# Kernel tuning notes

Hardware: AMD Instinct MI355X
Metric: run time of the kernel (lower is better)

The kernel has to match this reference:

```python
import jax, jax.numpy as jnp
import numpy as np

B, T, EMB_D, HEAD = 8, 2048, 1024, 128


def setup_inputs() -> dict:
    key = jax.random.key(0)
    ks = jax.random.split(key, 7)
    s = 1.0 / np.sqrt(EMB_D)
    return {
        "inputs": jax.random.normal(ks[0], (B, T, EMB_D), dtype=jnp.float32),
        "Wk": jax.random.uniform(ks[1], (EMB_D, HEAD), jnp.float32, -s, s),
        "bk": jax.random.uniform(ks[2], (HEAD,), jnp.float32, -s, s),
        "Wq": jax.random.uniform(ks[3], (EMB_D, HEAD), jnp.float32, -s, s),
        "bq": jax.random.uniform(ks[4], (HEAD,), jnp.float32, -s, s),
        "Wv": jax.random.uniform(ks[5], (EMB_D, HEAD), jnp.float32, -s, s),
        "bv": jax.random.uniform(ks[6], (HEAD,), jnp.float32, -s, s),
    }


def reference(inputs, Wk, bk, Wq, bq, Wv, bv):
    # inputs: [B, T, C]
    Bq, Tq, _ = inputs.shape
    k = inputs @ Wk + bk  # [B, T, H]
    q = inputs @ Wq + bq
    v = inputs @ Wv + bv
    scale = HEAD ** -0.5
    weights = jnp.einsum("bth,bsh->bts", q, k) * scale  # [B, T, T]
    causal = jnp.tril(jnp.ones((Tq, Tq), dtype=bool))
    weights = jnp.where(causal, weights, -jnp.inf)
    # NOTE: original code applies softmax over dim=1 (the query axis), faithfully reproduced
    weights = jax.nn.softmax(weights, axis=1)
    return jnp.einsum("bts,bsh->bth", weights, v)  # [B, T, H]
```

## Files before the change

kernel.cpp:

```cpp
#include <hip/hip_runtime.h>
#include <hip/hip_bf16.h>

#define T_SEQ 2048
#define NBATCH 8
#define EMB 1024
#define HD 128

typedef _Float16 f16_t;
typedef _Float16 f16x8 __attribute__((ext_vector_type(8)));
typedef _Float16 f16x4 __attribute__((ext_vector_type(4)));
typedef float f32x4 __attribute__((ext_vector_type(4)));


__device__ __forceinline__ void g2l(const f16_t* g, f16_t* l) {
    __builtin_amdgcn_global_load_lds(
        (const __attribute__((address_space(1))) unsigned int*)g,
        (__attribute__((address_space(3))) unsigned int*)l, 16, 0, 0);
}

__global__ __launch_bounds__(256) void prep(
    const float* __restrict__ Wk, const float* __restrict__ bk,
    const float* __restrict__ Wq, const float* __restrict__ bq,
    const float* __restrict__ Wv, const float* __restrict__ bv,
    f16_t* __restrict__ w2, float* __restrict__ biasc,
    float4* __restrict__ out4, float4* __restrict__ colsum4) {
    int bid = blockIdx.x;
    int t = threadIdx.x;
    if (bid < 384) {
        int n = bid;
        const float scale = 0.08838834764831845f;
        const float* W; const float* bias; float sc; int col;
        if (n < 128)      { W = Wq; bias = bq; sc = scale; col = n; }
        else if (n < 256) { W = Wk; bias = bk; sc = 1.0f;  col = n - 128; }
        else              { W = Wv; bias = bv; sc = 1.0f;  col = n - 256; }
        if (t < 128) {
            int k0 = t * 8;
            f16x8 v;
            #pragma unroll
            for (int i = 0; i < 8; ++i) v[i] = (f16_t)(W[(size_t)(k0 + i) * HD + col] * sc);
            *(f16x8*)&w2[(size_t)(n >> 4) * 16384 + (size_t)(k0 >> 3) * 128 + (n & 15) * 8] = v;
        }
        if (t == 0) biasc[n] = bias[col] * sc;
    } else if (bid < 384 + 2048) {
        out4[(size_t)(bid - 384) * 256 + t] = make_float4(0.f, 0.f, 0.f, 0.f);
    } else {
        colsum4[(size_t)(bid - 2432) * 256 + t] = make_float4(0.f, 0.f, 0.f, 0.f);
    }
}

__global__ __launch_bounds__(256) void qkv_gemm(
    const float* __restrict__ X, const f16_t* __restrict__ w2,
    const float* __restrict__ biasc,
    f16_t* __restrict__ q2, f16_t* __restrict__ k2, f16_t* __restrict__ v2) {
    __shared__ f16_t Xs[64 * 72];

    int bid = blockIdx.x;
    int r8 = bid & 7, g = bid >> 3;
    int band = (g / 3) * 8 + r8;
    int i = g % 3;
    int m0 = band * 64, n0 = i * 128;
    int tid = threadIdx.x;
    int lane = tid & 63, w = tid >> 6;
    int quad = lane >> 4, l15 = lane & 15;
    int msub = (w & 1) * 32, nsub = (w >> 1) * 64;

    int srow = tid >> 2;
    int scg  = (tid & 3) * 16;

    const float* xrow = X + (size_t)(m0 + srow) * EMB + scg;

    f32x4 acc[2][4] = {};
    float4 pfA[4], pfB[4];
    #pragma unroll
    for (int u = 0; u < 4; ++u) pfA[u] = *(const float4*)(xrow + u * 4);
    #pragma unroll
    for (int u = 0; u < 4; ++u) pfB[u] = *(const float4*)(xrow + 64 + u * 4);

    auto stage = [&](float4 (&pf)[4]) {
        union { f16_t h[8]; uint4 u4; } p0, p1;
        p0.h[0] = (f16_t)pf[0].x; p0.h[1] = (f16_t)pf[0].y;
        p0.h[2] = (f16_t)pf[0].z; p0.h[3] = (f16_t)pf[0].w;
        p0.h[4] = (f16_t)pf[1].x; p0.h[5] = (f16_t)pf[1].y;
        p0.h[6] = (f16_t)pf[1].z; p0.h[7] = (f16_t)pf[1].w;
        p1.h[0] = (f16_t)pf[2].x; p1.h[1] = (f16_t)pf[2].y;
        p1.h[2] = (f16_t)pf[2].z; p1.h[3] = (f16_t)pf[2].w;
        p1.h[4] = (f16_t)pf[3].x; p1.h[5] = (f16_t)pf[3].y;
        p1.h[6] = (f16_t)pf[3].z; p1.h[7] = (f16_t)pf[3].w;
        *(uint4*)&Xs[srow * 72 + scg] = p0.u4;
        *(uint4*)&Xs[srow * 72 + scg + 8] = p1.u4;
    };
    auto compute = [&](int kc) {
        #pragma unroll
        for (int ks = 0; ks < 2; ++ks) {
            f16x8 afr0 = *(const f16x8*)&Xs[(msub + l15) * 72 + ks * 32 + quad * 8];
            f16x8 afr1 = *(const f16x8*)&Xs[(msub + 16 + l15) * 72 + ks * 32 + quad * 8];
            #pragma unroll
            for (int nf = 0; nf < 4; ++nf) {
                int ntile = (n0 + nsub + nf * 16) >> 4;
                f16x8 bfr = *(const f16x8*)&w2[(size_t)ntile * 16384 +
                    (size_t)((kc >> 3) + ks * 4 + quad) * 128 + l15 * 8];
                acc[0][nf] = __builtin_amdgcn_mfma_f32_16x16x32_f16(afr0, bfr, acc[0][nf], 0, 0, 0);
                acc[1][nf] = __builtin_amdgcn_mfma_f32_16x16x32_f16(afr1, bfr, acc[1][nf], 0, 0, 0);
            }
        }
    };

    for (int it = 0; it < 16; it += 2) {
        __syncthreads();
        stage(pfA);
        __syncthreads();
        if (it + 2 < 16) {
            #pragma unroll
            for (int u = 0; u < 4; ++u) pfA[u] = *(const float4*)(xrow + (it + 2) * 64 + u * 4);
        }
        compute(it * 64);

        __syncthreads();
        stage(pfB);
        __syncthreads();
        if (it + 3 < 16) {
            #pragma unroll
            for (int u = 0; u < 4; ++u) pfB[u] = *(const float4*)(xrow + (it + 3) * 64 + u * 4);
        }
        compute((it + 1) * 64);
    }

    #pragma unroll
    for (int nf = 0; nf < 4; ++nf) {
        int ng = n0 + nsub + nf * 16 + l15;
        float bval = biasc[ng];
        #pragma unroll
        for (int mf = 0; mf < 2; ++mf) {
            int rowg = m0 + msub + mf * 16 + quad * 4;
            f32x4 a = acc[mf][nf];
            if (ng < 256) {
                f16_t* dst = (ng < 128) ? q2 : k2;
                int c = ng & 127;
                #pragma unroll
                for (int r = 0; r < 4; ++r) {
                    int row = rowg + r;
                    dst[(size_t)(row >> 4) * 2048 + (c >> 3) * 128 + (row & 15) * 8 + (c & 7)]
                        = (f16_t)(a[r] + bval);
                }
            } else {
                int h = ng - 256;
                f16x4 hv;
                #pragma unroll
                for (int r = 0; r < 4; ++r) hv[r] = (f16_t)(a[r] + bval);
                *(f16x4*)&v2[(size_t)(rowg >> 3) * 1024 + h * 8 + (rowg & 7)] = hv;
            }
        }
    }
}

__global__ __launch_bounds__(256, 4) void col_stats(
    const f16_t* __restrict__ q2, const f16_t* __restrict__ k2,
    float* __restrict__ colsum) {
    __shared__ __align__(16) f16_t Ql[4 * 2048];

    int bid = blockIdx.x;
    int b = bid & 7;
    int item = 143 - (bid >> 3);
    int cg = 0, slab = 0, cum = 0;
    for (int c = 0; c < 32; ++c) {
        int n = (32 - c + 3) >> 2;
        if (item < cum + n) { cg = c; slab = item - cum; break; }
        cum += n;
    }
    int tc0 = cg + slab * 4, tc1 = min(tc0 + 4, 32);

    int tid = threadIdx.x, lane = tid & 63, w = tid >> 6;
    int quad = lane >> 4, l15 = lane & 15;
    int brow = b * 128;
    size_t base = (size_t)b * T_SEQ;

    f16x8 bfrs[4][4];
    #pragma unroll
    for (int st = 0; st < 4; ++st) {
        const f16_t* kt = k2 + (size_t)(brow + cg * 4 + st) * 2048 + l15 * 8;
        #pragma unroll
        for (int kf = 0; kf < 4; ++kf)
            bfrs[st][kf] = *(const f16x8*)(kt + (kf * 4 + quad) * 128);
    }

    float lacc[4] = {0.f, 0.f, 0.f, 0.f};

    for (int tc = tc0; tc < tc1; ++tc) {
        int tb = tc * 64;
        __syncthreads();
        const f16_t* qsrc = q2 + (size_t)(brow + tc * 4) * 2048;
        #pragma unroll
        for (int i = 0; i < 4; ++i)
            g2l(qsrc + i * 2048 + tid * 8, Ql + i * 2048 + tid * 8);
        __syncthreads();

        f16x8 afr[4];
        #pragma unroll
        for (int kf = 0; kf < 4; ++kf)
            afr[kf] = *(const f16x8*)&Ql[w * 2048 + (kf * 4 + quad) * 128 + l15 * 8];
        #pragma unroll
        for (int st = 0; st < 4; ++st) {
            f32x4 s = {};
            #pragma unroll
            for (int kf = 0; kf < 4; ++kf)
                s = __builtin_amdgcn_mfma_f32_16x16x32_f16(afr[kf], bfrs[st][kf], s, 0, 0, 0);
            int scol = cg * 64 + st * 16 + l15;
            #pragma unroll
            for (int r = 0; r < 4; ++r) {
                int t = tb + w * 16 + quad * 4 + r;
                if (t >= scol) lacc[st] += __expf(s[r]);
            }
        }
    }

    #pragma unroll
    for (int st = 0; st < 4; ++st) {
        float v = lacc[st];
        v += __shfl_xor(v, 16, 64);
        v += __shfl_xor(v, 32, 64);
        if (quad == 0) atomicAdd(&colsum[base + cg * 64 + st * 16 + l15], v);
    }
}

__global__ __launch_bounds__(256, 4) void attn_out(
    const f16_t* __restrict__ q2, const f16_t* __restrict__ k2,
    const f16_t* __restrict__ v2, const float* __restrict__ colsum,
    float* __restrict__ out) {
    __shared__ __align__(16) f16_t Kl[4 * 2048];
    __shared__ __align__(16) f16_t Vl[8 * 1024];
    __shared__ __align__(16) f16_t Pl[32 * 72];

    int bid = blockIdx.x;
    int b = bid & 7;
    int item = 159 - (bid >> 3);
    int g = 0, slab = 0, cum = 0;
    for (int gg = 0; gg < 64; ++gg) {
        int n = (((gg >> 1) + 1) + 7) >> 3;
        if (item < cum + n) { g = gg; slab = item - cum; break; }
        cum += n;
    }
    int nch = (g >> 1) + 1;
    int c0 = slab * 8, c1 = min(c0 + 8, nch);
    int trow = g * 32;

    int tid = threadIdx.x, lane = tid & 63, w = tid >> 6;
    int quad = lane >> 4, l15 = lane & 15;
    int brow = b * 128;
    size_t base = (size_t)b * T_SEQ;

    f16x8 qfr[2][4];
    #pragma unroll
    for (int tt = 0; tt < 2; ++tt) {
        const f16_t* qt = q2 + (size_t)(brow + 2 * g + tt) * 2048 + l15 * 8;
        #pragma unroll
        for (int kf = 0; kf < 4; ++kf)
            qfr[tt][kf] = *(const f16x8*)(qt + (kf * 4 + quad) * 128);
    }

    f32x4 o[2][2] = {};

    for (int c = c0; c < c1; ++c) {
        int sb = c * 64;
        __syncthreads();
        const f16_t* ksrc = k2 + (size_t)(brow + (sb >> 4)) * 2048;
        const f16_t* vsrc = v2 + (((size_t)base + sb) >> 3) * 1024;
        #pragma unroll
        for (int i = 0; i < 4; ++i) {
            g2l(ksrc + i * 2048 + tid * 8, Kl + i * 2048 + tid * 8);
            g2l(vsrc + i * 2048 + tid * 8, Vl + i * 2048 + tid * 8);
        }
        __syncthreads();

        float iv = 1.0f / colsum[base + sb + w * 16 + l15];
        int scol = sb + w * 16 + l15;
        f16x8 bfr[4];
        #pragma unroll
        for (int kf = 0; kf < 4; ++kf)
            bfr[kf] = *(const f16x8*)&Kl[w * 2048 + (kf * 4 + quad) * 128 + l15 * 8];
        #pragma unroll
        for (int tt = 0; tt < 2; ++tt) {
            f32x4 s = {};
            #pragma unroll
            for (int kf = 0; kf < 4; ++kf)
                s = __builtin_amdgcn_mfma_f32_16x16x32_f16(qfr[tt][kf], bfr[kf], s, 0, 0, 0);
            #pragma unroll
            for (int r = 0; r < 4; ++r) {
                int t = trow + tt * 16 + quad * 4 + r;
                float pv = (t >= scol) ? __expf(s[r]) * iv : 0.f;
                Pl[(tt * 16 + quad * 4 + r) * 72 + w * 16 + l15] = (f16_t)pv;
            }
        }
        __syncthreads();

        #pragma unroll
        for (int kf2 = 0; kf2 < 2; ++kf2) {
            f16x8 pa0 = *(const f16x8*)&Pl[(l15) * 72 + kf2 * 32 + quad * 8];
            f16x8 pa1 = *(const f16x8*)&Pl[(16 + l15) * 72 + kf2 * 32 + quad * 8];
            #pragma unroll
            for (int hh = 0; hh < 2; ++hh) {
                f16x8 vfr = *(const f16x8*)&Vl[(kf2 * 4 + quad) * 1024 + (w * 32 + hh * 16 + l15) * 8];
                o[0][hh] = __builtin_amdgcn_mfma_f32_16x16x32_f16(pa0, vfr, o[0][hh], 0, 0, 0);
                o[1][hh] = __builtin_amdgcn_mfma_f32_16x16x32_f16(pa1, vfr, o[1][hh], 0, 0, 0);
            }
        }
    }

    #pragma unroll
    for (int tt = 0; tt < 2; ++tt)
        #pragma unroll
        for (int hh = 0; hh < 2; ++hh)
            #pragma unroll
            for (int r = 0; r < 4; ++r)
                atomicAdd(&out[(base + trow + tt * 16 + quad * 4 + r) * HD + w * 32 + hh * 16 + l15],
                          o[tt][hh][r]);
}

extern "C" void kernel_launch(void* const* d_in, const int* in_sizes, int n_in,
                              void* d_out, int out_size, void* d_ws, size_t ws_size,
                              hipStream_t stream) {
    const float* X  = (const float*)d_in[0];
    const float* Wk = (const float*)d_in[1];
    const float* bk = (const float*)d_in[2];
    const float* Wq = (const float*)d_in[3];
    const float* bq = (const float*)d_in[4];
    const float* Wv = (const float*)d_in[5];
    const float* bv = (const float*)d_in[6];
    float* out = (float*)d_out;

    char* ws = (char*)d_ws;
    const size_t W2_B    = 24 * 16384 * 2;
    const size_t BIAS_B  = 2048;
    const size_t QKV_B   = (size_t)NBATCH * T_SEQ * HD * 2;
    f16_t* w2     = (f16_t*)ws;
    float* biasc  = (float*)(ws + W2_B);
    f16_t* q2     = (f16_t*)(ws + W2_B + BIAS_B);
    f16_t* k2     = (f16_t*)(ws + W2_B + BIAS_B + QKV_B);
    f16_t* v2     = (f16_t*)(ws + W2_B + BIAS_B + 2 * QKV_B);
    float* colsum = (float*)(ws + W2_B + BIAS_B + 3 * QKV_B);

    prep<<<dim3(2448), dim3(256), 0, stream>>>(Wk, bk, Wq, bq, Wv, bv, w2, biasc,
                                               (float4*)out, (float4*)colsum);
    qkv_gemm<<<dim3(768), dim3(256), 0, stream>>>(X, w2, biasc, q2, k2, v2);
    col_stats<<<dim3(1152), dim3(256), 0, stream>>>(q2, k2, colsum);
    attn_out<<<dim3(1280), dim3(256), 0, stream>>>(q2, k2, v2, colsum, out);
}
```

Measured before the change: 176.1 us.

## Stream fp32 X tiles via direct global-to-LDS loads with XOR swizzle and double buffering

After: 177.4 us. Within noise of the previous version (+0.7%).

```diff
diff --git a/kernel.cpp b/kernel.cpp
--- a/kernel.cpp
+++ b/kernel.cpp
@@ -12,7 +12,7 @@
 typedef float f32x4 __attribute__((ext_vector_type(4)));
 
 
-__device__ __forceinline__ void g2l(const f16_t* g, f16_t* l) {
+__device__ __forceinline__ void g2l(const void* g, void* l) {
     __builtin_amdgcn_global_load_lds(
         (const __attribute__((address_space(1))) unsigned int*)g,
         (__attribute__((address_space(3))) unsigned int*)l, 16, 0, 0);
@@ -48,81 +48,72 @@
     }
 }
 
-__global__ __launch_bounds__(256) void qkv_gemm(
+__global__ __launch_bounds__(256, 3) void qkv_gemm(
     const float* __restrict__ X, const f16_t* __restrict__ w2,
     const float* __restrict__ biasc,
     f16_t* __restrict__ q2, f16_t* __restrict__ k2, f16_t* __restrict__ v2) {
-    __shared__ f16_t Xs[64 * 72];
+    __shared__ __align__(16) float Xs[2][4096];
 
     int bid = blockIdx.x;
-    int r8 = bid & 7, g = bid >> 3;
-    int band = (g / 3) * 8 + r8;
-    int i = g % 3;
-    int m0 = band * 64, n0 = i * 128;
+    int r8 = bid & 7, gb = bid >> 3;
+    int band = (gb / 3) * 8 + r8;
+    int csib = gb % 3;
+    int m0 = band * 64, n0 = csib * 128;
     int tid = threadIdx.x;
     int lane = tid & 63, w = tid >> 6;
     int quad = lane >> 4, l15 = lane & 15;
     int msub = (w & 1) * 32, nsub = (w >> 1) * 64;
 
-    int srow = tid >> 2;
-    int scg  = (tid & 3) * 16;
-
-    const float* xrow = X + (size_t)(m0 + srow) * EMB + scg;
+    int rr = tid >> 4;
+    int gg = (tid & 15) ^ rr;
+    const float* xbase = X + (size_t)(m0 + rr) * EMB + gg * 4;
 
     f32x4 acc[2][4] = {};
-    float4 pfA[4], pfB[4];
-    #pragma unroll
-    for (int u = 0; u < 4; ++u) pfA[u] = *(const float4*)(xrow + u * 4);
-    #pragma unroll
-    for (int u = 0; u < 4; ++u) pfB[u] = *(const float4*)(xrow + 64 + u * 4);
-
-    auto stage = [&](float4 (&pf)[4]) {
-        union { f16_t h[8]; uint4 u4; } p0, p1;
-        p0.h[0] = (f16_t)pf[0].x; p0.h[1] = (f16_t)pf[0].y;
-        p0.h[2] = (f16_t)pf[0].z; p0.h[3] = (f16_t)pf[0].w;
-        p0.h[4] = (f16_t)pf[1].x; p0.h[5] = (f16_t)pf[1].y;
-        p0.h[6] = (f16_t)pf[1].z; p0.h[7] = (f16_t)pf[1].w;
-        p1.h[0] = (f16_t)pf[2].x; p1.h[1] = (f16_t)pf[2].y;
-        p1.h[2] = (f16_t)pf[2].z; p1.h[3] = (f16_t)pf[2].w;
-        p1.h[4] = (f16_t)pf[3].x; p1.h[5] = (f16_t)pf[3].y;
-        p1.h[6] = (f16_t)pf[3].z; p1.h[7] = (f16_t)pf[3].w;
-        *(uint4*)&Xs[srow * 72 + scg] = p0.u4;
-        *(uint4*)&Xs[srow * 72 + scg + 8] = p1.u4;
-    };
-    auto compute = [&](int kc) {
-        #pragma unroll
-        for (int ks = 0; ks < 2; ++ks) {
-            f16x8 afr0 = *(const f16x8*)&Xs[(msub + l15) * 72 + ks * 32 + quad * 8];
-            f16x8 afr1 = *(const f16x8*)&Xs[(msub + 16 + l15) * 72 + ks * 32 + quad * 8];
+
+    #pragma unroll
+    for (int ii = 0; ii < 4; ++ii)
+        g2l(xbase + (size_t)ii * 16 * EMB, &Xs[0][(ii * 256 + tid) * 4]);
+
+    for (int it = 0; it < 16; ++it) {
+        __builtin_amdgcn_s_waitcnt(0);
+        __syncthreads();
+        int cur = it & 1;
+
+        f16x8 bfr[2][4];
+        #pragma unroll
+        for (int ks = 0; ks < 2; ++ks)
             #pragma unroll
             for (int nf = 0; nf < 4; ++nf) {
                 int ntile = (n0 + nsub + nf * 16) >> 4;
-                f16x8 bfr = *(const f16x8*)&w2[(size_t)ntile * 16384 +
-                    (size_t)((kc >> 3) + ks * 4 + quad) * 128 + l15 * 8];
-                acc[0][nf] = __builtin_amdgcn_mfma_f32_16x16x32_f16(afr0, bfr, acc[0][nf], 0, 0, 0);
-                acc[1][nf] = __builtin_amdgcn_mfma_f32_16x16x32_f16(afr1, bfr, acc[1][nf], 0, 0, 0);
-            }
-        }
-    };
-
-    for (int it = 0; it < 16; it += 2) {
-        __syncthreads();
-        stage(pfA);
-        __syncthreads();
-        if (it + 2 < 16) {
-            #pragma unroll
-            for (int u = 0; u < 4; ++u) pfA[u] = *(const float4*)(xrow + (it + 2) * 64 + u * 4);
-        }
-        compute(it * 64);
-
-        __syncthreads();
-        stage(pfB);
-        __syncthreads();
-        if (it + 3 < 16) {
-            #pragma unroll
-            for (int u = 0; u < 4; ++u) pfB[u] = *(const float4*)(xrow + (it + 3) * 64 + u * 4);
-        }
-        compute((it + 1) * 64);
+                bfr[ks][nf] = *(const f16x8*)&w2[(size_t)ntile * 16384 +
+                    (size_t)(it * 8 + ks * 4 + quad) * 128 + l15 * 8];
+            }
+
+        if (it + 1 < 16) {
+            const float* src = xbase + (it + 1) * 64;
+            #pragma unroll
+            for (int ii = 0; ii < 4; ++ii)
+                g2l(src + (size_t)ii * 16 * EMB, &Xs[cur ^ 1][(ii * 256 + tid) * 4]);
+        }
+
+        #pragma unroll
+        for (int ks = 0; ks < 2; ++ks) {
+            int g0 = ks * 8 + quad * 2;
+            #pragma unroll
+            for (int mf = 0; mf < 2; ++mf) {
+                int rl = msub + mf * 16 + l15;
+                float4 fa = *(const float4*)&Xs[cur][(rl * 16 + (g0 ^ l15)) * 4];
+                float4 fb = *(const float4*)&Xs[cur][(rl * 16 + ((g0 + 1) ^ l15)) * 4];
+                f16x8 afr;
+                afr[0] = (f16_t)fa.x; afr[1] = (f16_t)fa.y;
+                afr[2] = (f16_t)fa.z; afr[3] = (f16_t)fa.w;
+                afr[4] = (f16_t)fb.x; afr[5] = (f16_t)fb.y;
+                afr[6] = (f16_t)fb.z; afr[7] = (f16_t)fb.w;
+                #pragma unroll
+                for (int nf = 0; nf < 4; ++nf)
+                    acc[mf][nf] = __builtin_amdgcn_mfma_f32_16x16x32_f16(afr, bfr[ks][nf], acc[mf][nf], 0, 0, 0);
+            }
+        }
     }
 
     #pragma unroll
@@ -191,7 +182,7 @@
         const f16_t* qsrc = q2 + (size_t)(brow + tc * 4) * 2048;
         #pragma unroll
         for (int i = 0; i < 4; ++i)
-            g2l(qsrc + i * 2048 + tid * 8, Ql + i * 2048 + tid * 8);
+            g2l(qsrc + i * 2048 + tid * 8, &Ql[i * 2048 + tid * 8]);
         __syncthreads();
 
         f16x8 afr[4];
@@ -266,8 +257,8 @@
         const f16_t* vsrc = v2 + (((size_t)base + sb) >> 3) * 1024;
         #pragma unroll
         for (int i = 0; i < 4; ++i) {
-            g2l(ksrc + i * 2048 + tid * 8, Kl + i * 2048 + tid * 8);
-            g2l(vsrc + i * 2048 + tid * 8, Vl + i * 2048 + tid * 8);
+            g2l(ksrc + i * 2048 + tid * 8, &Kl[i * 2048 + tid * 8]);
+            g2l(vsrc + i * 2048 + tid * 8, &Vl[i * 2048 + tid * 8]);
         }
         __syncthreads();
 
```
